# Kernel tuning notes

Hardware: AMD Instinct MI355X
Metric: run time of the kernel (lower is better)

The kernel has to match this reference:

```python
import jax, jax.numpy as jnp
import numpy as np

D_MODEL = 1024
N_HEADS = 16
HEAD_DIM = D_MODEL // N_HEADS
WINDOW = 128  # radius w; attend to [i-w, i+w]


def setup_inputs() -> dict:
    key = jax.random.key(0)
    ks = jax.random.split(key, 5)
    scale = 1.0 / np.sqrt(D_MODEL)
    x = jax.random.normal(ks[0], (2, 2048, D_MODEL), dtype=jnp.float32)
    # nn.MultiheadAttention packed projections
    in_proj_w = jax.random.normal(ks[1], (3 * D_MODEL, D_MODEL), dtype=jnp.float32) * scale
    in_proj_b = jnp.zeros((3 * D_MODEL,), dtype=jnp.float32)
    out_w = jax.random.normal(ks[2], (D_MODEL, D_MODEL), dtype=jnp.float32) * scale
    out_b = jnp.zeros((D_MODEL,), dtype=jnp.float32)
    return {"x": x, "in_proj_w": in_proj_w, "in_proj_b": in_proj_b,
            "out_w": out_w, "out_b": out_b}


def reference(x, in_proj_w, in_proj_b, out_w, out_b):
    B, S, D = x.shape
    H, Dh = N_HEADS, HEAD_DIM
    # packed qkv projection (PyTorch: x @ W^T + b)
    qkv = x @ in_proj_w.T + in_proj_b              # [B, S, 3D]
    q, k, v = jnp.split(qkv, 3, axis=-1)
    q = q.reshape(B, S, H, Dh)
    k = k.reshape(B, S, H, Dh)
    v = v.reshape(B, S, H, Dh)
    scores = jnp.einsum('bqhd,bkhd->bhqk', q, k) / np.sqrt(Dh)  # [B,H,S,S]
    # window mask: allowed iff |i - j| <= WINDOW
    idx = jnp.arange(S)
    allowed = jnp.abs(idx[:, None] - idx[None, :]) <= WINDOW    # [S, S]
    scores = jnp.where(allowed[None, None], scores, -jnp.inf)
    attn = jax.nn.softmax(scores, axis=-1)
    out = jnp.einsum('bhqk,bkhd->bqhd', attn, v).reshape(B, S, D)
    return out @ out_w.T + out_b
```

## Files before the change

kernel.cpp:

```cpp
#include <hip/hip_runtime.h>


#define S_LEN 2048
#define NH 16
#define DH 64
#define DM 1024
#define WIN 128

typedef __attribute__((ext_vector_type(8))) short short8;
typedef __attribute__((ext_vector_type(4))) short short4_t;
typedef __attribute__((ext_vector_type(4))) float f32x4;
typedef __attribute__((ext_vector_type(16))) float f32x16;

__device__ __forceinline__ unsigned short f2bf(float f){
  unsigned u = __float_as_uint(f);
  u += 0x7fffu + ((u >> 16) & 1u);
  return (unsigned short)(u >> 16);
}
__device__ __forceinline__ unsigned pk2(float lo, float hi){
  return (unsigned)f2bf(lo) | ((unsigned)f2bf(hi) << 16);
}

__device__ __forceinline__ void async16(void* l, const void* g){
  __builtin_amdgcn_global_load_lds((const __attribute__((address_space(1))) void*)g,
                                   (__attribute__((address_space(3))) void*)l, 16, 0, 0);
}

__global__ void cvt_bf16(const float* __restrict__ in, short* __restrict__ out, int n){
  int i = (blockIdx.x * blockDim.x + threadIdx.x) * 4;
  if (i >= n) return;
  float4 v = *(const float4*)(in + i);
  short4_t o;
  o.x = (short)f2bf(v.x); o.y = (short)f2bf(v.y);
  o.z = (short)f2bf(v.z); o.w = (short)f2bf(v.w);
  *(short4_t*)(out + i) = o;
}

__global__ __launch_bounds__(256) void gemm_qkv(
    const short* __restrict__ A, const short* __restrict__ Bw,
    const float* __restrict__ bias,
    short* __restrict__ Qb, short* __restrict__ Kb, short* __restrict__ Vb)
{
  __shared__ short As[128*32], Bs[128*32];
  const int K = 1024;
  int tid = threadIdx.x;
  int lane = tid & 63, wv = tid >> 6;
  int wr = wv >> 1, wc = wv & 1;
  int lr = lane & 15, lh = lane >> 4;
  int m0 = blockIdx.y * 128, n0 = blockIdx.x * 128;

  f32x4 acc[4][4] = {};
  for (int kt = 0; kt < K; kt += 32) {
    #pragma unroll
    for (int i = 0; i < 2; ++i) {
      int c = i*256 + tid;
      int row = c >> 2, col = (c & 3) << 3;
      async16(&As[c*8], A  + (size_t)(m0+row)*K + kt + col);
      async16(&Bs[c*8], Bw + (size_t)(n0+row)*K + kt + col);
    }
    __syncthreads();
    short8 af[4], bfr[4];
    #pragma unroll
    for (int m = 0; m < 4; ++m) af[m]  = *(const short8*)&As[(wr*64 + m*16 + lr)*32 + lh*8];
    #pragma unroll
    for (int n = 0; n < 4; ++n) bfr[n] = *(const short8*)&Bs[(wc*64 + n*16 + lr)*32 + lh*8];
    #pragma unroll
    for (int m = 0; m < 4; ++m)
      #pragma unroll
      for (int n = 0; n < 4; ++n)
        acc[m][n] = __builtin_amdgcn_mfma_f32_16x16x32_bf16(af[m], bfr[n], acc[m][n], 0, 0, 0);
    __syncthreads();
  }
  #pragma unroll
  for (int m = 0; m < 4; ++m) {
    #pragma unroll
    for (int n = 0; n < 4; ++n) {
      int col = n0 + wc*64 + n*16 + lr;
      float bv = bias[col];
      int which = col >> 10, cc = col & 1023;
      int h = cc >> 6, d = cc & 63;
      float scl = which == 0 ? 0.125f : 1.0f;
      #pragma unroll
      for (int r = 0; r < 4; ++r) {
        int grow = m0 + wr*64 + m*16 + lh*4 + r;
        int b = grow >> 11, s = grow & 2047;
        float v = (acc[m][n][r] + bv) * scl;
        if (which == 2) {
          Vb[((size_t)(b*NH + h)*DH + d)*S_LEN + s] = (short)f2bf(v);
        } else {
          short* dst = which == 0 ? Qb : Kb;
          dst[(((size_t)b*NH + h)*S_LEN + s)*DH + d] = (short)f2bf(v);
        }
      }
    }
  }
}

__global__ __launch_bounds__(256) void gemm_out(
    const short* __restrict__ A, const short* __restrict__ Bw,
    const float* __restrict__ bias, float* __restrict__ Out)
{
  __shared__ short As[128*32], Bs[128*32];
  const int K = 1024;
  int tid = threadIdx.x;
  int lane = tid & 63, wv = tid >> 6;
  int wr = wv >> 1, wc = wv & 1;
  int lr = lane & 15, lh = lane >> 4;
  int m0 = blockIdx.y * 128, n0 = blockIdx.x * 128;

  f32x4 acc[4][4] = {};
  for (int kt = 0; kt < K; kt += 32) {
    #pragma unroll
    for (int i = 0; i < 2; ++i) {
      int c = i*256 + tid;
      int row = c >> 2, col = (c & 3) << 3;
      async16(&As[c*8], A  + (size_t)(m0+row)*K + kt + col);
      async16(&Bs[c*8], Bw + (size_t)(n0+row)*K + kt + col);
    }
    __syncthreads();
    short8 af[4], bfr[4];
    #pragma unroll
    for (int m = 0; m < 4; ++m) af[m]  = *(const short8*)&As[(wr*64 + m*16 + lr)*32 + lh*8];
    #pragma unroll
    for (int n = 0; n < 4; ++n) bfr[n] = *(const short8*)&Bs[(wc*64 + n*16 + lr)*32 + lh*8];
    #pragma unroll
    for (int m = 0; m < 4; ++m)
      #pragma unroll
      for (int n = 0; n < 4; ++n)
        acc[m][n] = __builtin_amdgcn_mfma_f32_16x16x32_bf16(af[m], bfr[n], acc[m][n], 0, 0, 0);
    __syncthreads();
  }
  #pragma unroll
  for (int m = 0; m < 4; ++m) {
    #pragma unroll
    for (int n = 0; n < 4; ++n) {
      int col = n0 + wc*64 + n*16 + lr;
      float bv = bias[col];
      #pragma unroll
      for (int r = 0; r < 4; ++r) {
        int grow = m0 + wr*64 + m*16 + lh*4 + r;
        Out[(size_t)grow*DM + col] = acc[m][n][r] + bv;
      }
    }
  }
}

__global__ __launch_bounds__(256) void attn_mfma(
    const short* __restrict__ Qb, const short* __restrict__ Kb,
    const short* __restrict__ VTb, short* __restrict__ Ob)
{
  int tid = threadIdx.x;
  int lane = tid & 63, wv = tid >> 6;
  int q31 = lane & 31, h2 = lane >> 5;
  int bh = blockIdx.y;
  int q0w = blockIdx.x * 128 + wv * 32;
  int qa = q0w + q31;

  const short* Qg = Qb  + (size_t)bh * S_LEN * DH;
  const short* Kg = Kb  + (size_t)bh * S_LEN * DH;
  const short* Vg = VTb + (size_t)bh * DH * S_LEN;

  short8 qf[4];
  #pragma unroll
  for (int kc = 0; kc < 4; ++kc)
    qf[kc] = *(const short8*)(Qg + (size_t)qa * DH + kc*16 + h2*8);

  int ks = q0w - WIN; if (ks < 0) ks = 0;
  int ke = q0w + 32 + WIN; if (ke > S_LEN) ke = S_LEN;

  f32x16 o0 = {}, o1 = {};
  float m = -1e37f, l = 0.f;

  for (int t0 = ks; t0 < ke; t0 += 32) {
    f32x16 s = {};
    #pragma unroll
    for (int kc = 0; kc < 4; ++kc) {
      short8 kf = *(const short8*)(Kg + (size_t)(t0 + q31) * DH + kc*16 + h2*8);
      s = __builtin_amdgcn_mfma_f32_32x32x16_bf16(kf, qf[kc], s, 0, 0, 0);
    }
    float p[16];
    float tm = -1e38f;
    #pragma unroll
    for (int r = 0; r < 16; ++r) {
      int key = t0 + (r & 3) + 8*(r >> 2) + 4*h2;
      bool ok = (key >= qa - WIN) && (key <= qa + WIN);
      p[r] = ok ? s[r] : -1e38f;
      tm = fmaxf(tm, p[r]);
    }
    tm = fmaxf(tm, __shfl_xor(tm, 32, 64));
    float mn = fmaxf(m, tm);
    float sc = __expf(m - mn);
    float ts = 0.f;
    #pragma unroll
    for (int r = 0; r < 16; ++r) { p[r] = __expf(p[r] - mn); ts += p[r]; }
    ts += __shfl_xor(ts, 32, 64);
    l = l * sc + ts;
    m = mn;
    #pragma unroll
    for (int r = 0; r < 16; ++r) { o0[r] *= sc; o1[r] *= sc; }

    #pragma unroll
    for (int kc2 = 0; kc2 < 2; ++kc2) {
      unsigned A1 = pk2(p[kc2*8+0], p[kc2*8+1]);
      unsigned A2 = pk2(p[kc2*8+2], p[kc2*8+3]);
      unsigned B1 = pk2(p[kc2*8+4], p[kc2*8+5]);
      unsigned B2 = pk2(p[kc2*8+6], p[kc2*8+7]);
      unsigned sA1 = (unsigned)__shfl_xor((int)A1, 32, 64);
      unsigned sA2 = (unsigned)__shfl_xor((int)A2, 32, 64);
      unsigned sB1 = (unsigned)__shfl_xor((int)B1, 32, 64);
      unsigned sB2 = (unsigned)__shfl_xor((int)B2, 32, 64);
      union { unsigned u[4]; short8 v; } pa;
      pa.u[0] = h2 ? sB1 : A1;
      pa.u[1] = h2 ? sB2 : A2;
      pa.u[2] = h2 ? B1 : sA1;
      pa.u[3] = h2 ? B2 : sA2;
      #pragma unroll
      for (int mt = 0; mt < 2; ++mt) {
        short8 vf = *(const short8*)(Vg + (size_t)(mt*32 + q31) * S_LEN + t0 + kc2*16 + h2*8);
        if (mt == 0) o0 = __builtin_amdgcn_mfma_f32_32x32x16_bf16(vf, pa.v, o0, 0, 0, 0);
        else         o1 = __builtin_amdgcn_mfma_f32_32x32x16_bf16(vf, pa.v, o1, 0, 0, 0);
      }
    }
  }

  float inv = 1.0f / l;
  int b = bh >> 4, hh = bh & 15;
  unsigned* Orow = (unsigned*)Ob + ((size_t)b*S_LEN + qa) * (DM/2) + hh*32;
  #pragma unroll
  for (int mt = 0; mt < 2; ++mt) {
    #pragma unroll
    for (int a = 0; a < 4; ++a) {
      #pragma unroll
      for (int e = 0; e < 2; ++e) {
        int r = 4*a + 2*e;
        float x0 = (mt ? o1[r]   : o0[r])   * inv;
        float x1 = (mt ? o1[r+1] : o0[r+1]) * inv;
        int d = 2*e + 8*a + 4*h2 + 32*mt;
        Orow[d >> 1] = pk2(x0, x1);
      }
    }
  }
}

extern "C" void kernel_launch(void* const* d_in, const int* in_sizes, int n_in,
                              void* d_out, int out_size, void* d_ws, size_t ws_size,
                              hipStream_t stream) {
  const float* x  = (const float*)d_in[0];
  const float* w1 = (const float*)d_in[1];
  const float* b1 = (const float*)d_in[2];
  const float* wo = (const float*)d_in[3];
  const float* bo = (const float*)d_in[4];
  float* out = (float*)d_out;

  char* ws = (char*)d_ws;
  short* xb  = (short*)(ws);
  short* w1b = (short*)(ws + (size_t)8*1024*1024);
  short* wob = (short*)(ws + (size_t)14*1024*1024);
  short* Qb  = (short*)(ws + (size_t)16*1024*1024);
  short* Kb  = (short*)(ws + (size_t)24*1024*1024);
  short* VTb = (short*)(ws + (size_t)32*1024*1024);
  short* Ab  = (short*)(ws + (size_t)40*1024*1024);

  cvt_bf16<<<dim3(4096), dim3(256), 0, stream>>>(x,  xb,  2*2048*1024);
  cvt_bf16<<<dim3(3072), dim3(256), 0, stream>>>(w1, w1b, 3072*1024);
  cvt_bf16<<<dim3(1024), dim3(256), 0, stream>>>(wo, wob, 1024*1024);
  gemm_qkv<<<dim3(24, 32), dim3(256), 0, stream>>>(xb, w1b, b1, Qb, Kb, VTb);
  attn_mfma<<<dim3(16, 32), dim3(256), 0, stream>>>(Qb, Kb, VTb, Ab);
  gemm_out<<<dim3(8, 32), dim3(256), 0, stream>>>(Ab, wob, bo, out);
}
```

Before: 173.2 us.

## Rewrite QKV GEMM with 256x256 tiles, double-buffered swizzled LDS and interleaved MFMA

Replaces the 128x128 single-buffered QKV projection GEMM with a 512-thread kernel using 256x256 output tiles and a K step of 64. A/B half-tiles are staged into double-buffered LDS with an XOR swizzle to avoid bank conflicts, and each load stage is interleaved with MFMA quarter-blocks under fine-grained barriers, vmcnt waits and raised wave priority. The aim is more data reuse per LDS load and overlap of global-to-LDS copies with matrix math. The cost is 128KB of LDS per block and only 192 blocks, which leaves some CUs idle.

```diff
diff --git a/kernel.cpp b/kernel.cpp
--- a/kernel.cpp
+++ b/kernel.cpp
@@ -6,6 +6,7 @@
 #define DH 64
 #define DM 1024
 #define WIN 128
+#define K_DIM 1024
 
 typedef __attribute__((ext_vector_type(8))) short short8;
 typedef __attribute__((ext_vector_type(4))) short short4_t;
@@ -20,11 +21,15 @@
 __device__ __forceinline__ unsigned pk2(float lo, float hi){
   return (unsigned)f2bf(lo) | ((unsigned)f2bf(hi) << 16);
 }
-
 __device__ __forceinline__ void async16(void* l, const void* g){
   __builtin_amdgcn_global_load_lds((const __attribute__((address_space(1))) void*)g,
                                    (__attribute__((address_space(3))) void*)l, 16, 0, 0);
 }
+
+#define FENCE asm volatile("" ::: "memory")
+#define BAR   do { FENCE; __builtin_amdgcn_s_barrier(); FENCE; } while(0)
+#define WAITV6 asm volatile("s_waitcnt vmcnt(6)" ::: "memory")
+#define WAITV0 asm volatile("s_waitcnt vmcnt(0)" ::: "memory")
 
 __global__ void cvt_bf16(const float* __restrict__ in, short* __restrict__ out, int n){
   int i = (blockIdx.x * blockDim.x + threadIdx.x) * 4;
@@ -36,43 +41,111 @@
   *(short4_t*)(out + i) = o;
 }
 
-__global__ __launch_bounds__(256) void gemm_qkv(
+__device__ __forceinline__ void stageA(short* ldsA, const short* A, int m0, int T, int H, int tid){
+  #pragma unroll
+  for (int j = 0; j < 2; ++j) {
+    int off16 = j*512 + tid;
+    int lrow = off16 >> 3, slin = off16 & 7;
+    int g = (lrow & 63) + ((lrow >> 6) << 7) + H*64;
+    int sg = slin ^ (lrow & 7);
+    async16(ldsA + ((H*128 + lrow)*64 + slin*8),
+            A + (size_t)(m0 + g)*K_DIM + T*64 + sg*8);
+  }
+}
+__device__ __forceinline__ void stageB(short* ldsB, const short* Bw, int n0, int T, int H, int tid){
+  #pragma unroll
+  for (int j = 0; j < 2; ++j) {
+    int off16 = j*512 + tid;
+    int lrow = off16 >> 3, slin = off16 & 7;
+    int g = ((lrow >> 5) << 6) + H*32 + (lrow & 31);
+    int sg = slin ^ (lrow & 7);
+    async16(ldsB + ((H*128 + lrow)*64 + slin*8),
+            Bw + (size_t)(n0 + g)*K_DIM + T*64 + sg*8);
+  }
+}
+__device__ __forceinline__ void ldA(const short* At, int wr, int lr, int lh, int mq, short8 a[4][2]){
+  #pragma unroll
+  for (int mm = 0; mm < 4; ++mm)
+    #pragma unroll
+    for (int kk = 0; kk < 2; ++kk)
+      a[mm][kk] = *(const short8*)(At + (mq*128 + wr*64 + mm*16 + lr)*64 + (((kk*4 + lh) ^ (lr & 7))*8));
+}
+__device__ __forceinline__ void ldB(const short* Bt, int wc, int lr, int lh, int nq, short8 b[2][2]){
+  #pragma unroll
+  for (int nn = 0; nn < 2; ++nn)
+    #pragma unroll
+    for (int kk = 0; kk < 2; ++kk)
+      b[nn][kk] = *(const short8*)(Bt + (nq*128 + wc*32 + nn*16 + lr)*64 + (((kk*4 + lh) ^ (lr & 7))*8));
+}
+__device__ __forceinline__ void mfma8(f32x4 acc[8][4], const short8 a[4][2], const short8 b[2][2], int mq, int nq){
+  __builtin_amdgcn_s_setprio(1);
+  #pragma unroll
+  for (int mm = 0; mm < 4; ++mm)
+    #pragma unroll
+    for (int nn = 0; nn < 2; ++nn)
+      #pragma unroll
+      for (int kk = 0; kk < 2; ++kk)
+        acc[mq*4+mm][nq*2+nn] =
+          __builtin_amdgcn_mfma_f32_16x16x32_bf16(a[mm][kk], b[nn][kk], acc[mq*4+mm][nq*2+nn], 0, 0, 0);
+  __builtin_amdgcn_s_setprio(0);
+}
+
+__global__ __launch_bounds__(512, 2) void gemm_qkv8(
     const short* __restrict__ A, const short* __restrict__ Bw,
     const float* __restrict__ bias,
     short* __restrict__ Qb, short* __restrict__ Kb, short* __restrict__ Vb)
 {
-  __shared__ short As[128*32], Bs[128*32];
-  const int K = 1024;
-  int tid = threadIdx.x;
-  int lane = tid & 63, wv = tid >> 6;
-  int wr = wv >> 1, wc = wv & 1;
-  int lr = lane & 15, lh = lane >> 4;
-  int m0 = blockIdx.y * 128, n0 = blockIdx.x * 128;
-
-  f32x4 acc[4][4] = {};
-  for (int kt = 0; kt < K; kt += 32) {
-    #pragma unroll
-    for (int i = 0; i < 2; ++i) {
-      int c = i*256 + tid;
-      int row = c >> 2, col = (c & 3) << 3;
-      async16(&As[c*8], A  + (size_t)(m0+row)*K + kt + col);
-      async16(&Bs[c*8], Bw + (size_t)(n0+row)*K + kt + col);
-    }
-    __syncthreads();
-    short8 af[4], bfr[4];
-    #pragma unroll
-    for (int m = 0; m < 4; ++m) af[m]  = *(const short8*)&As[(wr*64 + m*16 + lr)*32 + lh*8];
-    #pragma unroll
-    for (int n = 0; n < 4; ++n) bfr[n] = *(const short8*)&Bs[(wc*64 + n*16 + lr)*32 + lh*8];
-    #pragma unroll
-    for (int m = 0; m < 4; ++m)
-      #pragma unroll
-      for (int n = 0; n < 4; ++n)
-        acc[m][n] = __builtin_amdgcn_mfma_f32_16x16x32_bf16(af[m], bfr[n], acc[m][n], 0, 0, 0);
-    __syncthreads();
-  }
-  #pragma unroll
-  for (int m = 0; m < 4; ++m) {
+  __shared__ short lds[65536];
+  short* A0 = lds;          short* A1 = lds + 16384;
+  short* B0 = lds + 32768;  short* B1 = lds + 49152;
+  int tid = threadIdx.x, lane = tid & 63, wid = tid >> 6;
+  int wr = wid >> 2, wc = wid & 3, lr = lane & 15, lh = lane >> 4;
+  int m0 = blockIdx.y * 256, n0 = blockIdx.x * 256;
+
+  f32x4 acc[8][4] = {};
+  short8 a[4][2], b0[2][2], b1[2][2];
+
+  stageA(A0, A, m0, 0, 0, tid);
+  stageA(A0, A, m0, 0, 1, tid);
+  stageB(B0, Bw, n0, 0, 0, tid);
+  stageB(B0, Bw, n0, 0, 1, tid);
+  stageA(A1, A, m0, 1, 0, tid);
+  stageB(B1, Bw, n0, 1, 0, tid);
+  stageB(B1, Bw, n0, 1, 1, tid);
+  WAITV6; BAR;
+
+  for (int i = 0; i < 8; ++i) {
+    int t1 = 2*i + 1, t2 = 2*i + 2, t3 = 2*i + 3;
+    bool more = (i < 7);
+    ldA(A0, wr, lr, lh, 0, a); ldB(B0, wc, lr, lh, 0, b0);
+    stageA(A1, A, m0, t1, 1, tid);
+    BAR; mfma8(acc, a, b0, 0, 0); BAR;
+    ldB(B0, wc, lr, lh, 1, b1);
+    if (more) stageA(A0, A, m0, t2, 0, tid);
+    BAR; mfma8(acc, a, b1, 0, 1); BAR;
+    ldA(A0, wr, lr, lh, 1, a);
+    if (more) stageB(B0, Bw, n0, t2, 0, tid);
+    BAR; mfma8(acc, a, b1, 1, 1); BAR;
+    if (more) stageB(B0, Bw, n0, t2, 1, tid);
+    BAR; mfma8(acc, a, b0, 1, 0);
+    if (more) { WAITV6; } else { WAITV0; }
+    BAR;
+    ldA(A1, wr, lr, lh, 0, a); ldB(B1, wc, lr, lh, 0, b0);
+    if (more) stageA(A0, A, m0, t2, 1, tid);
+    BAR; mfma8(acc, a, b0, 0, 0); BAR;
+    ldB(B1, wc, lr, lh, 1, b1);
+    if (more) stageA(A1, A, m0, t3, 0, tid);
+    BAR; mfma8(acc, a, b1, 0, 1); BAR;
+    ldA(A1, wr, lr, lh, 1, a);
+    if (more) stageB(B1, Bw, n0, t3, 0, tid);
+    BAR; mfma8(acc, a, b1, 1, 1); BAR;
+    if (more) stageB(B1, Bw, n0, t3, 1, tid);
+    BAR; mfma8(acc, a, b0, 1, 0);
+    WAITV6; BAR;
+  }
+
+  #pragma unroll
+  for (int m = 0; m < 8; ++m) {
     #pragma unroll
     for (int n = 0; n < 4; ++n) {
       int col = n0 + wc*64 + n*16 + lr;
@@ -82,14 +155,14 @@
       float scl = which == 0 ? 0.125f : 1.0f;
       #pragma unroll
       for (int r = 0; r < 4; ++r) {
-        int grow = m0 + wr*64 + m*16 + lh*4 + r;
-        int b = grow >> 11, s = grow & 2047;
+        int grow = m0 + wr*128 + m*16 + lh*4 + r;
+        int bb = grow >> 11, s = grow & 2047;
         float v = (acc[m][n][r] + bv) * scl;
         if (which == 2) {
-          Vb[((size_t)(b*NH + h)*DH + d)*S_LEN + s] = (short)f2bf(v);
+          Vb[((size_t)(bb*NH + h)*DH + d)*S_LEN + s] = (short)f2bf(v);
         } else {
           short* dst = which == 0 ? Qb : Kb;
-          dst[(((size_t)b*NH + h)*S_LEN + s)*DH + d] = (short)f2bf(v);
+          dst[(((size_t)bb*NH + h)*S_LEN + s)*DH + d] = (short)f2bf(v);
         }
       }
     }
@@ -101,7 +174,6 @@
     const float* __restrict__ bias, float* __restrict__ Out)
 {
   __shared__ short As[128*32], Bs[128*32];
-  const int K = 1024;
   int tid = threadIdx.x;
   int lane = tid & 63, wv = tid >> 6;
   int wr = wv >> 1, wc = wv & 1;
@@ -109,13 +181,13 @@
   int m0 = blockIdx.y * 128, n0 = blockIdx.x * 128;
 
   f32x4 acc[4][4] = {};
-  for (int kt = 0; kt < K; kt += 32) {
+  for (int kt = 0; kt < K_DIM; kt += 32) {
     #pragma unroll
     for (int i = 0; i < 2; ++i) {
       int c = i*256 + tid;
       int row = c >> 2, col = (c & 3) << 3;
-      async16(&As[c*8], A  + (size_t)(m0+row)*K + kt + col);
-      async16(&Bs[c*8], Bw + (size_t)(n0+row)*K + kt + col);
+      async16(&As[c*8], A  + (size_t)(m0+row)*K_DIM + kt + col);
+      async16(&Bs[c*8], Bw + (size_t)(n0+row)*K_DIM + kt + col);
     }
     __syncthreads();
     short8 af[4], bfr[4];
@@ -229,13 +301,13 @@
   #pragma unroll
   for (int mt = 0; mt < 2; ++mt) {
     #pragma unroll
-    for (int a = 0; a < 4; ++a) {
+    for (int aa = 0; aa < 4; ++aa) {
       #pragma unroll
       for (int e = 0; e < 2; ++e) {
-        int r = 4*a + 2*e;
+        int r = 4*aa + 2*e;
         float x0 = (mt ? o1[r]   : o0[r])   * inv;
         float x1 = (mt ? o1[r+1] : o0[r+1]) * inv;
-        int d = 2*e + 8*a + 4*h2 + 32*mt;
+        int d = 2*e + 8*aa + 4*h2 + 32*mt;
         Orow[d >> 1] = pk2(x0, x1);
       }
     }
@@ -264,7 +336,7 @@
   cvt_bf16<<<dim3(4096), dim3(256), 0, stream>>>(x,  xb,  2*2048*1024);
   cvt_bf16<<<dim3(3072), dim3(256), 0, stream>>>(w1, w1b, 3072*1024);
   cvt_bf16<<<dim3(1024), dim3(256), 0, stream>>>(wo, wob, 1024*1024);
-  gemm_qkv<<<dim3(24, 32), dim3(256), 0, stream>>>(xb, w1b, b1, Qb, Kb, VTb);
+  gemm_qkv8<<<dim3(12, 16), dim3(512), 0, stream>>>(xb, w1b, b1, Qb, Kb, VTb);
   attn_mfma<<<dim3(16, 32), dim3(256), 0, stream>>>(Qb, Kb, VTb, Ab);
   gemm_out<<<dim3(8, 32), dim3(256), 0, stream>>>(Ab, wob, bo, out);
 }
```

New measurement: 188.4 us. +8.8%, slower.
